# Kernel optimization log

Hardware: AMD Instinct MI355X
Metric: run time of the kernel (lower is better)

## Reference

```python
import jax, jax.numpy as jnp
import numpy as np

NGRAMS = 5


def _pair_idx():
    pairs = [(i, j) for i in range(NGRAMS) for j in range(i + 1, NGRAMS)]
    return (np.array([p[0] for p in pairs]), np.array([p[1] for p in pairs]))


def setup_inputs() -> dict:
    key = jax.random.key(0)
    ks = jax.random.split(key, 12)
    B, S, U = 8, 500, 128
    n = NGRAMS
    C = S // n          # 100 chunks
    F = n * (n - 1)     # 2 * C(n,2) = 20 edge-concat feature width
    H, DK = n, 2        # per-chunk MHA: 5 heads, key_dim=value_dim=2
    GH, GD = 4, U // 4  # graph MHA: 4 heads, key_dim=32
    s = 0.05
    inp = {
        'x': jax.random.normal(ks[0], (B, S, U), jnp.float32),
        'wq': s * jax.random.normal(ks[1], (C, F, H, DK), jnp.float32),
        'bq': jnp.zeros((C, H, DK), jnp.float32),
        'wk': s * jax.random.normal(ks[2], (C, F, H, DK), jnp.float32),
        'bk': jnp.zeros((C, H, DK), jnp.float32),
        'wv': s * jax.random.normal(ks[3], (C, F, H, DK), jnp.float32),
        'bv': jnp.zeros((C, H, DK), jnp.float32),
        'wo': s * jax.random.normal(ks[4], (C, H, DK, F), jnp.float32),
        'bo': jnp.zeros((C, F), jnp.float32),
        'pos': 0.02 * jax.random.normal(ks[5], (C, U), jnp.float32),
        'gwq': s * jax.random.normal(ks[6], (U, GH, GD), jnp.float32),
        'gbq': jnp.zeros((GH, GD), jnp.float32),
        'gwk': s * jax.random.normal(ks[7], (U, GH, GD), jnp.float32),
        'gbk': jnp.zeros((GH, GD), jnp.float32),
        'gwv': s * jax.random.normal(ks[8], (U, GH, GD), jnp.float32),
        'gbv': jnp.zeros((GH, GD), jnp.float32),
        'gwo': s * jax.random.normal(ks[9], (GH, GD, U), jnp.float32),
        'gbo': jnp.zeros((U,), jnp.float32),
    }
    return inp


def reference(x, wq, bq, wk, bk, wv, bv, wo, bo, pos,
              gwq, gbq, gwk, gbk, gwv, gbv, gwo, gbo):
    B, S, U = x.shape
    n = NGRAMS
    C = S // n
    ii, jj = _pair_idx()
    P = ii.shape[0]
    # [B,S,U] -> [B,U,S] -> chunks [B,U,C,n]
    xt = jnp.transpose(x, (0, 2, 1)).reshape(B, U, C, n)
    # edge construction: concat of every node pair per chunk -> [B,U,C,2P]
    H_edges = jnp.stack([xt[..., ii], xt[..., jj]], axis=-1).reshape(B, U, C, 2 * P)
    Ht = jnp.transpose(H_edges, (0, 2, 1, 3))  # [B,C,U,F], attention seq axis = U
    dk = wq.shape[-1]
    scale = 1.0 / jnp.sqrt(jnp.asarray(dk, x.dtype))
    q = (jnp.einsum('bcuf,cfhd->bcuhd', Ht, wq) + bq[None, :, None]) * scale
    k = jnp.einsum('bcuf,cfhd->bcuhd', Ht, wk) + bk[None, :, None]
    v = jnp.einsum('bcuf,cfhd->bcuhd', Ht, wv) + bv[None, :, None]
    scores = jnp.einsum('bcuhd,bcvhd->bchuv', q, k)
    attn = jax.nn.softmax(scores, axis=-1)
    o = jnp.einsum('bchuv,bcvhd->bcuhd', attn, v)
    mha_out = jnp.einsum('bcuhd,chdf->bcuf', o, wo) + bo[None, :, None]
    alpha = jax.nn.leaky_relu(Ht + mha_out, negative_slope=0.3)  # [B,C,U,F]
    # stack + reduce_mean over edge-feature axis, transpose -> [B,C,U]
    g = jnp.mean(alpha, axis=-1)
    g = g + pos[None]  # learned position embedding over C
    # graph-level self-attention over the C axis
    gdk = gwq.shape[-1]
    gscale = 1.0 / jnp.sqrt(jnp.asarray(gdk, x.dtype))
    gq = (jnp.einsum('bcu,uhd->bchd', g, gwq) + gbq) * gscale
    gk = jnp.einsum('bcu,uhd->bchd', g, gwk) + gbk
    gv = jnp.einsum('bcu,uhd->bchd', g, gwv) + gbv
    gs = jnp.einsum('bqhd,bkhd->bhqk', gq, gk)
    ga = jax.nn.softmax(gs, axis=-1)
    go = jnp.einsum('bhqk,bkhd->bqhd', ga, gv)
    g_attn = jnp.einsum('bqhd,hdu->bqu', go, gwo) + gbo
    return g + g_attn  # [B, C, U]
```

## Files before the change

### kernel.cpp

```cpp
#include <hip/hip_runtime.h>

#define NB  8
#define SS  500
#define UU  128
#define NG  5
#define CC  100
#define FF  20
#define HH  5
#define HD  10

__device__ __constant__ const int EI[FF] =
    {0,1, 0,2, 0,3, 0,4, 1,2, 1,3, 1,4, 2,3, 2,4, 3,4};

__device__ __forceinline__ void proj10(const float* __restrict__ w,
                                       const float* __restrict__ bias,
                                       int c, const float xv[NG], float p[HD])
{
    const float2* bs2 = (const float2*)(bias + c * HD);
#pragma unroll
    for (int d2 = 0; d2 < 5; ++d2) {
        const float2 t2 = bs2[d2];
        p[2*d2] = t2.x; p[2*d2+1] = t2.y;
    }
    const float2* w2 = (const float2*)(w + c * (FF * HD));
#pragma unroll
    for (int f = 0; f < FF; ++f) {
        const float hf = xv[EI[f]];
#pragma unroll
        for (int d2 = 0; d2 < 5; ++d2) {
            const float2 t2 = w2[f*5 + d2];
            p[2*d2]   = fmaf(hf, t2.x, p[2*d2]);
            p[2*d2+1] = fmaf(hf, t2.y, p[2*d2+1]);
        }
    }
}

__global__ __launch_bounds__(512, 6) void k1_chunk_mha(
    const float* __restrict__ x,   const float* __restrict__ wq,
    const float* __restrict__ bq,  const float* __restrict__ wk,
    const float* __restrict__ bk,  const float* __restrict__ wv,
    const float* __restrict__ bv,  const float* __restrict__ wo,
    const float* __restrict__ bo,  const float* __restrict__ pos,
    const float* __restrict__ gwq, const float* __restrict__ gbq,
    const float* __restrict__ gwk, const float* __restrict__ gbk,
    const float* __restrict__ gwv, const float* __restrict__ gbv,
    float* __restrict__ g_out, float* __restrict__ gq_out,
    float* __restrict__ gk_out, float* __restrict__ gv_out)
{
    const int bc  = blockIdx.x;
    const int b   = bc / CC, c = bc % CC;
    const int tid = threadIdx.x;
    const int u   = tid & 127;
    const int vq  = tid >> 7;

    __shared__ float  s_q[HD][UU];
    __shared__ float4 s_kv[HH][UU];
    __shared__ float  s_g[UU];
    __shared__ float  s_part[4][HH*3][UU];
    float (*s_gr)[3][UU] = (float (*)[3][UU])s_part;

    float xv[NG];
    if (vq < 3) {
        const float* xb = x + (size_t)b * SS * UU + (size_t)c * NG * UU + u;
#pragma unroll
        for (int t = 0; t < NG; ++t) xv[t] = xb[t * UU];
    }
    if (vq == 0) {
        float p[HD];
        proj10(wq, bq, c, xv, p);
        const float scale = 0.7071067811865476f;
#pragma unroll
        for (int i = 0; i < HD; ++i) s_q[i][u] = p[i] * scale;
    } else if (vq == 1) {
        float p[HD];
        proj10(wk, bk, c, xv, p);
#pragma unroll
        for (int h = 0; h < HH; ++h) { s_kv[h][u].x = p[2*h]; s_kv[h][u].y = p[2*h+1]; }
    } else if (vq == 2) {
        float p[HD];
        proj10(wv, bv, c, xv, p);
#pragma unroll
        for (int h = 0; h < HH; ++h) { s_kv[h][u].z = p[2*h]; s_kv[h][u].w = p[2*h+1]; }
    }
    __syncthreads();

    float q0[HH], q1[HH];
#pragma unroll
    for (int h = 0; h < HH; ++h) { q0[h] = s_q[2*h][u]; q1[h] = s_q[2*h+1][u]; }
    float l[HH], o0[HH], o1[HH];
#pragma unroll
    for (int h = 0; h < HH; ++h) { l[h] = 0.f; o0[h] = 0.f; o1[h] = 0.f; }
    const int base = vq * 32;
#pragma unroll
    for (int h = 0; h < HH; ++h) {
#pragma unroll 8
        for (int i = 0; i < 32; ++i) {
            const float4 kv = s_kv[h][base + i];
            const float s = fmaf(q0[h], kv.x, q1[h] * kv.y);
            const float e = __expf(s);
            l[h] += e;
            o0[h] = fmaf(e, kv.z, o0[h]);
            o1[h] = fmaf(e, kv.w, o1[h]);
        }
    }
#pragma unroll
    for (int h = 0; h < HH; ++h) {
        s_part[vq][h*3+0][u] = l[h];
        s_part[vq][h*3+1][u] = o0[h];
        s_part[vq][h*3+2][u] = o1[h];
    }
    __syncthreads();

    if (vq == 0) {
        float o[HD];
#pragma unroll
        for (int h = 0; h < HH; ++h) {
            float L = 0.f, O0 = 0.f, O1 = 0.f;
#pragma unroll
            for (int j = 0; j < 4; ++j) {
                L  += s_part[j][h*3+0][u];
                O0 += s_part[j][h*3+1][u];
                O1 += s_part[j][h*3+2][u];
            }
            const float inv = 1.f / L;
            o[2*h] = O0 * inv; o[2*h+1] = O1 * inv;
        }
        const float* woc = wo + c * (HD * FF);
        const float* boc = bo + c * FF;
        float gsum = 0.f;
#pragma unroll
        for (int f = 0; f < FF; ++f) {
            float acc = boc[f];
#pragma unroll
            for (int hd = 0; hd < HD; ++hd) acc = fmaf(o[hd], woc[hd*FF + f], acc);
            const float a = xv[EI[f]] + acc;
            gsum += (a > 0.f) ? a : 0.3f * a;
        }
        const float g = gsum * (1.f / FF) + pos[c*UU + u];
        s_g[u] = g;
        g_out[(size_t)bc*UU + u] = g;
    }
    __syncthreads();

    float aq = 0.f, ak = 0.f, av = 0.f;
#pragma unroll 4
    for (int i = 0; i < 32; ++i) {
        const int u2 = vq*32 + i;
        const float gu = s_g[u2];
        aq = fmaf(gu, gwq[u2*UU + u], aq);
        ak = fmaf(gu, gwk[u2*UU + u], ak);
        av = fmaf(gu, gwv[u2*UU + u], av);
    }
    s_gr[vq][0][u] = aq; s_gr[vq][1][u] = ak; s_gr[vq][2][u] = av;
    __syncthreads();

    if (vq < 3) {
        const float s = s_gr[0][vq][u] + s_gr[1][vq][u]
                      + s_gr[2][vq][u] + s_gr[3][vq][u];
        if (vq == 0)
            gq_out[(size_t)bc*UU + u] = (s + gbq[u]) * 0.17677669529663687f;
        else if (vq == 1)
            gk_out[(size_t)bc*UU + u] = s + gbk[u];
        else
            gv_out[(size_t)bc*UU + u] = s + gbv[u];
    }
}

#define GHH 4
__global__ __launch_bounds__(256) void k2_graph(
    const float* __restrict__ gq, const float* __restrict__ gk,
    const float* __restrict__ gv, const float* __restrict__ gwo,
    const float* __restrict__ gbo, float* __restrict__ out)
{
    const int bq = blockIdx.x;
    const int b  = bq / CC;
    const int t  = threadIdx.x;

    __shared__ float s_q[UU];
    __shared__ float s_e[GHH][CC];
    __shared__ float s_pa[2][UU];
    __shared__ float s_pl[2][UU];
    __shared__ float s_o[UU];
    __shared__ float s_p3[2][UU];

    float gval = 0.f;
    if (t < UU) {
        gval  = out[(size_t)bq*UU + t];
        s_q[t] = gq[(size_t)bq*UU + t];
    }
    __syncthreads();

    if (t < 200) {
        const int k  = (t < 100) ? t : t - 100;
        const int h0 = (t < 100) ? 0 : 2;
        const float4* krow = (const float4*)(gk + ((size_t)b*CC + k)*UU);
        const float4* q4   = (const float4*)s_q;
#pragma unroll
        for (int hh = 0; hh < 2; ++hh) {
            const int h = h0 + hh;
            float s = 0.f;
#pragma unroll
            for (int i = 0; i < 8; ++i) {
                const float4 kf = krow[h*8 + i];
                const float4 qf = q4[h*8 + i];
                s = fmaf(qf.x, kf.x, s); s = fmaf(qf.y, kf.y, s);
                s = fmaf(qf.z, kf.z, s); s = fmaf(qf.w, kf.w, s);
            }
            s_e[h][k] = __expf(s);
        }
    }
    __syncthreads();

    {
        const int d = t & 127, kh = t >> 7, h = d >> 5;
        const float* vcol = gv + (size_t)b*CC*UU + d;
        float l = 0.f, o = 0.f;
#pragma unroll 5
        for (int i = 0; i < 50; ++i) {
            const int k = kh*50 + i;
            const float e = s_e[h][k];
            l += e;
            o = fmaf(e, vcol[(size_t)k*UU], o);
        }
        s_pa[kh][d] = o; s_pl[kh][d] = l;
    }
    __syncthreads();
    if (t < UU) s_o[t] = (s_pa[0][t] + s_pa[1][t]) / (s_pl[0][t] + s_pl[1][t]);
    __syncthreads();

    {
        const int u = t & 127, half = t >> 7;
        float acc = 0.f;
#pragma unroll 4
        for (int i = 0; i < 64; ++i) {
            const int hd = half*64 + i;
            acc = fmaf(s_o[hd], gwo[hd*UU + u], acc);
        }
        s_p3[half][u] = acc;
    }
    __syncthreads();
    if (t < UU)
        out[(size_t)bq*UU + t] = gval + s_p3[0][t] + s_p3[1][t] + gbo[t];
}

extern "C" void kernel_launch(void* const* d_in, const int* in_sizes, int n_in,
                              void* d_out, int out_size, void* d_ws, size_t ws_size,
                              hipStream_t stream)
{
    (void)in_sizes; (void)n_in; (void)out_size; (void)ws_size;
    const float* x   = (const float*)d_in[0];
    const float* wq  = (const float*)d_in[1];
    const float* bq  = (const float*)d_in[2];
    const float* wk  = (const float*)d_in[3];
    const float* bk  = (const float*)d_in[4];
    const float* wv  = (const float*)d_in[5];
    const float* bv  = (const float*)d_in[6];
    const float* wo  = (const float*)d_in[7];
    const float* bo  = (const float*)d_in[8];
    const float* pos = (const float*)d_in[9];
    const float* gwq = (const float*)d_in[10];
    const float* gbq = (const float*)d_in[11];
    const float* gwk = (const float*)d_in[12];
    const float* gbk = (const float*)d_in[13];
    const float* gwv = (const float*)d_in[14];
    const float* gbv = (const float*)d_in[15];
    const float* gwo = (const float*)d_in[16];
    const float* gbo = (const float*)d_in[17];
    float* out = (float*)d_out;
    float* ws  = (float*)d_ws;

    float* gq_ws = ws;
    float* gk_ws = ws + 102400;
    float* gv_ws = ws + 204800;

    k1_chunk_mha<<<NB*CC, 512, 0, stream>>>(x, wq, bq, wk, bk, wv, bv, wo, bo,
        pos, gwq, gbq, gwk, gbk, gwv, gbv, out, gq_ws, gk_ws, gv_ws);
    k2_graph<<<NB*CC, 256, 0, stream>>>(gq_ws, gk_ws, gv_ws, gwo, gbo, out);
}
```

Measured before the change: 129.7 us.

## Reduce chunk attention partials with DPP quad sums and compute output projection per-lane

Remaps the per-chunk attention so the four key-partition partials for each position sit in adjacent lanes and are combined with DPP quad reductions instead of going through shared memory and a barrier. Every thread now runs the output projection and leaky-relu mean redundantly, with only lane 0 of each quad writing the result, and x is staged in shared memory. Both softmax stages fold log2(e) into the query scale and use the native exp2 instruction. The occupancy hint on the first kernel is dropped. In exchange, the redundant per-lane output projection costs about four times the ALU work, and register pressure may rise.

```diff
diff --git a/kernel.cpp b/kernel.cpp
--- a/kernel.cpp
+++ b/kernel.cpp
@@ -8,9 +8,21 @@
 #define FF  20
 #define HH  5
 #define HD  10
+#define GHH 4
 
 __device__ __constant__ const int EI[FF] =
     {0,1, 0,2, 0,3, 0,4, 1,2, 1,3, 1,4, 2,3, 2,4, 3,4};
+
+template <int CTRL>
+__device__ __forceinline__ float qperm(float x) {
+    return __int_as_float(__builtin_amdgcn_update_dpp(
+        0, __float_as_int(x), CTRL, 0xF, 0xF, true));
+}
+__device__ __forceinline__ float quad_sum(float x) {
+    x += qperm<0xB1>(x);
+    x += qperm<0x4E>(x);
+    return x;
+}
 
 __device__ __forceinline__ void proj10(const float* __restrict__ w,
                                        const float* __restrict__ bias,
@@ -35,7 +47,7 @@
     }
 }
 
-__global__ __launch_bounds__(512, 6) void k1_chunk_mha(
+__global__ __launch_bounds__(512) void k1_chunk_mha(
     const float* __restrict__ x,   const float* __restrict__ wq,
     const float* __restrict__ bq,  const float* __restrict__ wk,
     const float* __restrict__ bk,  const float* __restrict__ wv,
@@ -50,93 +62,95 @@
     const int bc  = blockIdx.x;
     const int b   = bc / CC, c = bc % CC;
     const int tid = threadIdx.x;
-    const int u   = tid & 127;
-    const int vq  = tid >> 7;
-
-    __shared__ float  s_q[HD][UU];
+    const int u0  = tid & 127;
+    const int grp = tid >> 7;
+
+    __shared__ float2 s_q[HH][UU];
     __shared__ float4 s_kv[HH][UU];
+    __shared__ float  s_x[NG][UU];
     __shared__ float  s_g[UU];
-    __shared__ float  s_part[4][HH*3][UU];
-    float (*s_gr)[3][UU] = (float (*)[3][UU])s_part;
+    __shared__ float  s_gr[4][3][UU];
 
     float xv[NG];
-    if (vq < 3) {
-        const float* xb = x + (size_t)b * SS * UU + (size_t)c * NG * UU + u;
-#pragma unroll
-        for (int t = 0; t < NG; ++t) xv[t] = xb[t * UU];
-    }
-    if (vq == 0) {
+    {
+        const float* xb = x + (size_t)b*SS*UU + (size_t)c*NG*UU + u0;
+#pragma unroll
+        for (int t = 0; t < NG; ++t) xv[t] = xb[t*UU];
+    }
+    if (grp == 0) {
         float p[HD];
         proj10(wq, bq, c, xv, p);
-        const float scale = 0.7071067811865476f;
-#pragma unroll
-        for (int i = 0; i < HD; ++i) s_q[i][u] = p[i] * scale;
-    } else if (vq == 1) {
+        const float C = 1.0202559313584566f;
+#pragma unroll
+        for (int h = 0; h < HH; ++h)
+            s_q[h][u0] = make_float2(p[2*h]*C, p[2*h+1]*C);
+    } else if (grp == 1) {
         float p[HD];
         proj10(wk, bk, c, xv, p);
 #pragma unroll
-        for (int h = 0; h < HH; ++h) { s_kv[h][u].x = p[2*h]; s_kv[h][u].y = p[2*h+1]; }
-    } else if (vq == 2) {
+        for (int h = 0; h < HH; ++h) { s_kv[h][u0].x = p[2*h]; s_kv[h][u0].y = p[2*h+1]; }
+    } else if (grp == 2) {
         float p[HD];
         proj10(wv, bv, c, xv, p);
 #pragma unroll
-        for (int h = 0; h < HH; ++h) { s_kv[h][u].z = p[2*h]; s_kv[h][u].w = p[2*h+1]; }
-    }
-    __syncthreads();
-
+        for (int h = 0; h < HH; ++h) { s_kv[h][u0].z = p[2*h]; s_kv[h][u0].w = p[2*h+1]; }
+    } else {
+#pragma unroll
+        for (int t = 0; t < NG; ++t) s_x[t][u0] = xv[t];
+    }
+    __syncthreads();
+
+    const int u  = tid >> 2;
+    const int vq = tid & 3;
     float q0[HH], q1[HH];
 #pragma unroll
-    for (int h = 0; h < HH; ++h) { q0[h] = s_q[2*h][u]; q1[h] = s_q[2*h+1][u]; }
+    for (int h = 0; h < HH; ++h) {
+        const float2 qq = s_q[h][u];
+        q0[h] = qq.x; q1[h] = qq.y;
+    }
     float l[HH], o0[HH], o1[HH];
 #pragma unroll
-    for (int h = 0; h < HH; ++h) { l[h] = 0.f; o0[h] = 0.f; o1[h] = 0.f; }
-    const int base = vq * 32;
+    for (int h = 0; h < HH; ++h) { l[h]=0.f; o0[h]=0.f; o1[h]=0.f; }
+    const int rot = 9*vq;
 #pragma unroll
     for (int h = 0; h < HH; ++h) {
 #pragma unroll 8
         for (int i = 0; i < 32; ++i) {
-            const float4 kv = s_kv[h][base + i];
-            const float s = fmaf(q0[h], kv.x, q1[h] * kv.y);
-            const float e = __expf(s);
-            l[h] += e;
-            o0[h] = fmaf(e, kv.z, o0[h]);
-            o1[h] = fmaf(e, kv.w, o1[h]);
-        }
-    }
+            const int v = vq*32 + ((i + rot) & 31);
+            const float4 kv = s_kv[h][v];
+            const float s = fmaf(q0[h], kv.x, q1[h]*kv.y);
+            const float e = __builtin_amdgcn_exp2f(s);
+            l[h]  += e;
+            o0[h]  = fmaf(e, kv.z, o0[h]);
+            o1[h]  = fmaf(e, kv.w, o1[h]);
+        }
+    }
+    float o[HD];
 #pragma unroll
     for (int h = 0; h < HH; ++h) {
-        s_part[vq][h*3+0][u] = l[h];
-        s_part[vq][h*3+1][u] = o0[h];
-        s_part[vq][h*3+2][u] = o1[h];
-    }
-    __syncthreads();
-
+        const float L  = quad_sum(l[h]);
+        const float O0 = quad_sum(o0[h]);
+        const float O1 = quad_sum(o1[h]);
+        const float inv = 1.f / L;
+        o[2*h] = O0*inv; o[2*h+1] = O1*inv;
+    }
+
+    float xu[NG];
+#pragma unroll
+    for (int t = 0; t < NG; ++t) xu[t] = s_x[t][u];
+    const float* woc = wo + c*(HD*FF);
+    const float* boc = bo + c*FF;
+    float gsum = 0.f;
+#pragma unroll
+    for (int f = 0; f < FF; ++f) {
+        float acc = boc[f];
+#pragma unroll
+        for (int hd = 0; hd < HD; ++hd) acc = fmaf(o[hd], woc[hd*FF + f], acc);
+        const float a = xu[EI[f]] + acc;
+        gsum += (a > 0.f) ? a : 0.3f*a;
+    }
+    const float g = gsum*(1.f/FF) + pos[c*UU + u];
     if (vq == 0) {
-        float o[HD];
-#pragma unroll
-        for (int h = 0; h < HH; ++h) {
-            float L = 0.f, O0 = 0.f, O1 = 0.f;
-#pragma unroll
-            for (int j = 0; j < 4; ++j) {
-                L  += s_part[j][h*3+0][u];
-                O0 += s_part[j][h*3+1][u];
-                O1 += s_part[j][h*3+2][u];
-            }
-            const float inv = 1.f / L;
-            o[2*h] = O0 * inv; o[2*h+1] = O1 * inv;
-        }
-        const float* woc = wo + c * (HD * FF);
-        const float* boc = bo + c * FF;
-        float gsum = 0.f;
-#pragma unroll
-        for (int f = 0; f < FF; ++f) {
-            float acc = boc[f];
-#pragma unroll
-            for (int hd = 0; hd < HD; ++hd) acc = fmaf(o[hd], woc[hd*FF + f], acc);
-            const float a = xv[EI[f]] + acc;
-            gsum += (a > 0.f) ? a : 0.3f * a;
-        }
-        const float g = gsum * (1.f / FF) + pos[c*UU + u];
         s_g[u] = g;
         g_out[(size_t)bc*UU + u] = g;
     }
@@ -145,28 +159,27 @@
     float aq = 0.f, ak = 0.f, av = 0.f;
 #pragma unroll 4
     for (int i = 0; i < 32; ++i) {
-        const int u2 = vq*32 + i;
+        const int u2 = grp*32 + i;
         const float gu = s_g[u2];
-        aq = fmaf(gu, gwq[u2*UU + u], aq);
-        ak = fmaf(gu, gwk[u2*UU + u], ak);
-        av = fmaf(gu, gwv[u2*UU + u], av);
-    }
-    s_gr[vq][0][u] = aq; s_gr[vq][1][u] = ak; s_gr[vq][2][u] = av;
-    __syncthreads();
-
-    if (vq < 3) {
-        const float s = s_gr[0][vq][u] + s_gr[1][vq][u]
-                      + s_gr[2][vq][u] + s_gr[3][vq][u];
-        if (vq == 0)
-            gq_out[(size_t)bc*UU + u] = (s + gbq[u]) * 0.17677669529663687f;
-        else if (vq == 1)
-            gk_out[(size_t)bc*UU + u] = s + gbk[u];
+        aq = fmaf(gu, gwq[u2*UU + u0], aq);
+        ak = fmaf(gu, gwk[u2*UU + u0], ak);
+        av = fmaf(gu, gwv[u2*UU + u0], av);
+    }
+    s_gr[grp][0][u0] = aq; s_gr[grp][1][u0] = ak; s_gr[grp][2][u0] = av;
+    __syncthreads();
+
+    if (grp < 3) {
+        const float s = s_gr[0][grp][u0] + s_gr[1][grp][u0]
+                      + s_gr[2][grp][u0] + s_gr[3][grp][u0];
+        if (grp == 0)
+            gq_out[(size_t)bc*UU + u0] = (s + gbq[u0]) * 0.17677669529663687f;
+        else if (grp == 1)
+            gk_out[(size_t)bc*UU + u0] = s + gbk[u0];
         else
-            gv_out[(size_t)bc*UU + u] = s + gbv[u];
-    }
-}
-
-#define GHH 4
+            gv_out[(size_t)bc*UU + u0] = s + gbv[u0];
+    }
+}
+
 __global__ __launch_bounds__(256) void k2_graph(
     const float* __restrict__ gq, const float* __restrict__ gk,
     const float* __restrict__ gv, const float* __restrict__ gwo,
@@ -186,7 +199,7 @@
     float gval = 0.f;
     if (t < UU) {
         gval  = out[(size_t)bq*UU + t];
-        s_q[t] = gq[(size_t)bq*UU + t];
+        s_q[t] = gq[(size_t)bq*UU + t] * 1.4426950408889634f;
     }
     __syncthreads();
 
@@ -206,7 +219,7 @@
                 s = fmaf(qf.x, kf.x, s); s = fmaf(qf.y, kf.y, s);
                 s = fmaf(qf.z, kf.z, s); s = fmaf(qf.w, kf.w, s);
             }
-            s_e[h][k] = __expf(s);
+            s_e[h][k] = __builtin_amdgcn_exp2f(s);
         }
     }
     __syncthreads();
```

Result: slower. 133.9 us (+3.2%).
